# Kernel optimization log

Measured on AMD Instinct MI355X. Metric: run time of the kernel, lower is better.

Reference implementation:

```python
import jax, jax.numpy as jnp
import numpy as np

B = 4; IMG = 32; P = 2; C_IN = 3; H_DIM = 384; DEPTH = 8
GS = IMG // P; L = GS * GS
NSTATE = 16; KDIR = 4; DIN = 384; RANK = 24; MH = int(H_DIM * 4.0)
BOT = 128; NCLS = 1000; TFREQ = 256


def _silu(x):
    return x * jax.nn.sigmoid(x)


def _rms(x, w, eps=1e-6):
    return x * jax.lax.rsqrt(jnp.mean(x * x, -1, keepdims=True) + eps) * w


def _ln(x, w, b, eps=1e-5):
    mu = jnp.mean(x, -1, keepdims=True)
    v = jnp.mean((x - mu) ** 2, -1, keepdims=True)
    return (x - mu) * jax.lax.rsqrt(v + eps) * w + b


def _ln_na(x, eps=1e-6):
    mu = jnp.mean(x, -1, keepdims=True)
    v = jnp.mean((x - mu) ** 2, -1, keepdims=True)
    return (x - mu) * jax.lax.rsqrt(v + eps)


def _mod(x, shift, scale):
    return x * (1.0 + scale[:, None, :]) + shift[:, None, :]


def _ss2d(xin, in_w, conv_w, conv_b, xproj_w, dt_w, dt_b, A_logs, Ds, onorm_w, onorm_b, outp_w):
    Bb = xin.shape[0]
    z = xin @ in_w.T  # (B,L,DIN)
    z2d = z.reshape(Bb, GS, GS, DIN).transpose(0, 3, 1, 2)  # (B,DIN,H,W)
    z2d = jax.lax.conv_general_dilated(z2d, conv_w, (1, 1), 'SAME',
        feature_group_count=DIN, dimension_numbers=('NCHW', 'OIHW', 'NCHW'))
    z2d = _silu(z2d + conv_b[None, :, None, None])
    # cross_scan -> (B,K,DIN,L): row-major, reversed, col-major, reversed col-major
    s1 = z2d.reshape(Bb, DIN, L)
    s3 = z2d.transpose(0, 1, 3, 2).reshape(Bb, DIN, L)
    xs = jnp.stack([s1, s1[..., ::-1], s3, s3[..., ::-1]], axis=1)
    x_dbl = jnp.einsum('bkdl,kod->bkol', xs, xproj_w)
    dtr = x_dbl[:, :, :RANK]
    Bssm = x_dbl[:, :, RANK:RANK + NSTATE]   # (B,K,N,L)
    Cssm = x_dbl[:, :, RANK + NSTATE:]       # (B,K,N,L)
    dt = jnp.einsum('bkrl,kdr->bkdl', dtr, dt_w)
    dt = jax.nn.softplus(dt + dt_b[None, :, :, None])
    A = -jnp.exp(A_logs)                     # (K,DIN,N)
    dA = jnp.exp(jnp.einsum('bkdl,kdn->bkldn', dt, A))
    dBu = jnp.einsum('bkdl,bknl->bkldn', dt * xs, Bssm)
    def comb(e1, e2):
        a1, b1 = e1
        a2, b2 = e2
        return a1 * a2, a2 * b1 + b2
    _, hs = jax.lax.associative_scan(comb, (dA, dBu), axis=2)  # h over token axis
    ys = jnp.einsum('bkldn,bknl->bkdl', hs, Cssm) + Ds[None, :, :, None] * xs
    # cross_merge: undo each direction's reorder and sum
    m1 = ys[:, 0]
    m2 = ys[:, 1][..., ::-1]
    m3 = ys[:, 2].reshape(Bb, DIN, GS, GS).swapaxes(2, 3).reshape(Bb, DIN, L)
    m4 = ys[:, 3][..., ::-1].reshape(Bb, DIN, GS, GS).swapaxes(2, 3).reshape(Bb, DIN, L)
    out = (m1 + m2 + m3 + m4).transpose(0, 2, 1)  # (B,L,DIN)
    out = _ln(out, onorm_w, onorm_b)
    return out @ outp_w.T


def _forward(x, t, y, t_w1, t_b1, t_w2, t_b2, y_table, pe_w1, pe_w2, pe_b2, pos_embed,
             adaln_w, adaln_b, n1_w, n2_w, in_w, conv_w, conv_b, xproj_w, dt_w, dt_b,
             A_logs, Ds, onorm_w, onorm_b, outp_w, mlp_w1, mlp_b1, mlp_w2, mlp_b2,
             f_adaln_w, f_adaln_b, f_lin_w, f_lin_b):
    # timestep embedding (DiT TimestepEmbedder, freq dim 256)
    half = TFREQ // 2
    freqs = jnp.exp(-jnp.log(10000.0) * jnp.arange(half, dtype=jnp.float32) / half)
    ang = t[:, None] * freqs[None]
    temb = jnp.concatenate([jnp.cos(ang), jnp.sin(ang)], axis=-1)
    temb = _silu(temb @ t_w1.T + t_b1) @ t_w2.T + t_b2
    c = temb + y_table[y]  # (B,H_DIM)
    # bottleneck patch embed: patchify -> bottleneck linear -> hidden linear
    xp = x.reshape(B, C_IN, GS, P, GS, P).transpose(0, 2, 4, 1, 3, 5).reshape(B, L, C_IN * P * P)
    h = (xp @ pe_w1.T) @ pe_w2.T + pe_b2
    h = h + pos_embed
    for i in range(DEPTH):
        mod = _silu(c) @ adaln_w[i].T + adaln_b[i]
        sh1, sc1, g1, sh2, sc2, g2 = jnp.split(mod, 6, axis=-1)
        h = h + g1[:, None] * _ss2d(_mod(_rms(h, n1_w[i]), sh1, sc1),
            in_w[i], conv_w[i], conv_b[i], xproj_w[i], dt_w[i], dt_b[i],
            A_logs[i], Ds[i], onorm_w[i], onorm_b[i], outp_w[i])
        u = _mod(_rms(h, n2_w[i]), sh2, sc2)
        u12 = u @ mlp_w1[i].T + mlp_b1[i]
        u1, u2 = jnp.split(u12, 2, axis=-1)
        h = h + g2[:, None] * ((_silu(u1) * u2) @ mlp_w2[i].T + mlp_b2[i])
    modf = _silu(c) @ f_adaln_w.T + f_adaln_b
    shf, scf = jnp.split(modf, 2, axis=-1)
    h = _mod(_ln_na(h), shf, scf)
    out = h @ f_lin_w.T + f_lin_b  # (B,L,P*P*C_IN)
    out = out.reshape(B, GS, GS, P, P, C_IN)
    out = jnp.einsum('nhwpqc->nchpwq', out)
    return out.reshape(B, C_IN, IMG, IMG)


def _sincos_1d(dim, pos):
    omega = 1.0 / (10000.0 ** (np.arange(dim // 2, dtype=np.float64) / (dim / 2.0)))
    out = pos.reshape(-1)[:, None] * omega[None, :]
    return np.concatenate([np.sin(out), np.cos(out)], axis=1)


def _pos_embed_np(dim, gs):
    g = np.stack(np.meshgrid(np.arange(gs, dtype=np.float64), np.arange(gs, dtype=np.float64)), axis=0)
    return np.concatenate([_sincos_1d(dim // 2, g[0]), _sincos_1d(dim // 2, g[1])], axis=1).astype(np.float32)


def setup_inputs():
    key = jax.random.key(0)
    ks = iter(jax.random.split(key, 64))
    nrm = lambda shape, s=0.02: jax.random.normal(next(ks), shape, jnp.float32) * s
    d = {}
    d['x'] = jax.random.normal(next(ks), (B, C_IN, IMG, IMG), jnp.float32)
    d['t'] = jax.random.uniform(next(ks), (B,), jnp.float32) * 1000.0
    d['y'] = jax.random.randint(next(ks), (B,), 0, NCLS)
    d['t_w1'] = nrm((H_DIM, TFREQ)); d['t_b1'] = jnp.zeros((H_DIM,), jnp.float32)
    d['t_w2'] = nrm((H_DIM, H_DIM)); d['t_b2'] = jnp.zeros((H_DIM,), jnp.float32)
    d['y_table'] = nrm((NCLS, H_DIM))
    d['pe_w1'] = nrm((BOT, C_IN * P * P), 0.1)
    d['pe_w2'] = nrm((H_DIM, BOT), 0.1); d['pe_b2'] = jnp.zeros((H_DIM,), jnp.float32)
    d['pos_embed'] = jnp.asarray(_pos_embed_np(H_DIM, GS))[None]
    d['adaln_w'] = nrm((DEPTH, 6 * H_DIM, H_DIM)); d['adaln_b'] = jnp.zeros((DEPTH, 6 * H_DIM), jnp.float32)
    d['n1_w'] = jnp.ones((DEPTH, H_DIM), jnp.float32); d['n2_w'] = jnp.ones((DEPTH, H_DIM), jnp.float32)
    d['in_w'] = nrm((DEPTH, DIN, H_DIM), 0.05)
    d['conv_w'] = nrm((DEPTH, DIN, 1, 3, 3), 0.1); d['conv_b'] = jnp.zeros((DEPTH, DIN), jnp.float32)
    d['xproj_w'] = nrm((DEPTH, KDIR, RANK + 2 * NSTATE, DIN), 0.05)
    d['dt_w'] = nrm((DEPTH, KDIR, DIN, RANK), 0.1)
    d['dt_b'] = nrm((DEPTH, KDIR, DIN), 0.5)
    d['A_logs'] = jnp.tile(jnp.log(jnp.arange(1, NSTATE + 1, dtype=jnp.float32))[None, None, None, :], (DEPTH, KDIR, DIN, 1))
    d['Ds'] = jnp.ones((DEPTH, KDIR, DIN), jnp.float32)
    d['onorm_w'] = jnp.ones((DEPTH, DIN), jnp.float32); d['onorm_b'] = jnp.zeros((DEPTH, DIN), jnp.float32)
    d['outp_w'] = nrm((DEPTH, H_DIM, DIN), 0.05)
    d['mlp_w1'] = nrm((DEPTH, 2 * MH, H_DIM)); d['mlp_b1'] = jnp.zeros((DEPTH, 2 * MH), jnp.float32)
    d['mlp_w2'] = nrm((DEPTH, H_DIM, MH)); d['mlp_b2'] = jnp.zeros((DEPTH, H_DIM), jnp.float32)
    d['f_adaln_w'] = nrm((2 * H_DIM, H_DIM)); d['f_adaln_b'] = jnp.zeros((2 * H_DIM,), jnp.float32)
    d['f_lin_w'] = nrm((P * P * C_IN, H_DIM)); d['f_lin_b'] = jnp.zeros((P * P * C_IN,), jnp.float32)
    return d


def reference(x, t, y, t_w1, t_b1, t_w2, t_b2, y_table, pe_w1, pe_w2, pe_b2, pos_embed,
              adaln_w, adaln_b, n1_w, n2_w, in_w, conv_w, conv_b, xproj_w, dt_w, dt_b,
              A_logs, Ds, onorm_w, onorm_b, outp_w, mlp_w1, mlp_b1, mlp_w2, mlp_b2,
              f_adaln_w, f_adaln_b, f_lin_w, f_lin_b):
    return _forward(x, t, y, t_w1, t_b1, t_w2, t_b2, y_table, pe_w1, pe_w2, pe_b2, pos_embed,
                    adaln_w, adaln_b, n1_w, n2_w, in_w, conv_w, conv_b, xproj_w, dt_w, dt_b,
                    A_logs, Ds, onorm_w, onorm_b, outp_w, mlp_w1, mlp_b1, mlp_w2, mlp_b2,
                    f_adaln_w, f_adaln_b, f_lin_w, f_lin_b)
```

## Files before the change

### kernel.cpp

```cpp
#include <hip/hip_runtime.h>
#include <hip/hip_bf16.h>
#include <math.h>


#define DEV __device__ __forceinline__

typedef __bf16 bf16_t;
typedef __attribute__((ext_vector_type(8))) __bf16 bf16x8;
typedef __attribute__((ext_vector_type(4))) float f32x4;
typedef __attribute__((ext_vector_type(2))) _Float16 h2;

DEV float siluf(float x){ return x / (1.f + __expf(-x)); }
DEV float softplusf(float x){ return fmaxf(x, 0.f) + __logf(1.f + __expf(-fabsf(x))); }

DEV int perm_idx(int k, int l){
  switch(k & 3){
    case 0: return l;
    case 1: return 255 - l;
    case 2: return ((l & 15) << 4) | (l >> 4);
    default: { int r = 255 - l; return ((r & 15) << 4) | (r >> 4); }
  }
}

__global__ void k_cvt_layer(const float* __restrict__ inw, const float* __restrict__ outw,
                            const float* __restrict__ w1, const float* __restrict__ w2,
                            const float* __restrict__ xp, bf16_t* __restrict__ dst){
  int idx = (blockIdx.x*256 + threadIdx.x)*4;
  const float* src; int off;
  if (idx < 147456){ src = inw;  off = idx; }
  else if (idx < 294912){ src = outw; off = idx - 147456; }
  else if (idx < 1474560){
    int o = idx - 294912;
    int rowc = o / 384, col = o - rowc*384;
    int q = rowc >> 5, tt = rowc & 31;
    int srow = (tt < 16) ? (q*16 + tt) : (1536 + q*16 + (tt - 16));
    src = w1; off = srow*384 + col;
  }
  else if (idx < 2064384){ src = w2; off = idx - 1474560; }
  else { src = xp; off = idx - 2064384; }
  float4 v = *(const float4*)(src + off);
  union { bf16_t h[4]; uint2 u; } cv;
  cv.h[0] = (bf16_t)v.x; cv.h[1] = (bf16_t)v.y; cv.h[2] = (bf16_t)v.z; cv.h[3] = (bf16_t)v.w;
  *(uint2*)(dst + idx) = cv.u;
}

__global__ void k_cond(const float* __restrict__ t, const int* __restrict__ y,
                       const float* __restrict__ tw1, const float* __restrict__ tb1,
                       const float* __restrict__ tw2, const float* __restrict__ tb2,
                       const float* __restrict__ ytab, float* __restrict__ sc){
  int b = blockIdx.x; int o = threadIdx.x;
  __shared__ float temb[256]; __shared__ float h1[384];
  float tv = t[b];
  if (o < 128){
    float f = __expf(-logf(10000.f) * (float)o / 128.f);
    float a = tv * f;
    temb[o] = cosf(a); temb[128 + o] = sinf(a);
  }
  __syncthreads();
  float acc = tb1[o];
  for (int j = 0; j < 256; j++) acc += temb[j] * tw1[(size_t)o*256 + j];
  h1[o] = siluf(acc);
  __syncthreads();
  float acc2 = tb2[o];
  for (int j = 0; j < 384; j++) acc2 += h1[j] * tw2[(size_t)o*384 + j];
  float c = acc2 + ytab[(size_t)y[b]*384 + o];
  sc[b*384 + o] = siluf(c);
}

__global__ void k_patch(const float* __restrict__ x, const float* __restrict__ pw1,
                        const float* __restrict__ pw2, const float* __restrict__ pb2,
                        const float* __restrict__ pos, float* __restrict__ h){
  int bl = blockIdx.x; int b = bl >> 8; int l = bl & 255;
  int gh = l >> 4, gw = l & 15;
  __shared__ float xp[12]; __shared__ float tmp[128];
  int tid = threadIdx.x;
  if (tid < 12){
    int ci = tid >> 2, ph = (tid >> 1) & 1, pw = tid & 1;
    xp[tid] = x[((size_t)(b*3 + ci)*32 + gh*2 + ph)*32 + gw*2 + pw];
  }
  __syncthreads();
  if (tid < 128){
    float a = 0.f;
    #pragma unroll
    for (int k = 0; k < 12; k++) a += xp[k] * pw1[tid*12 + k];
    tmp[tid] = a;
  }
  __syncthreads();
  float a = pb2[tid];
  for (int j = 0; j < 128; j++) a += tmp[j] * pw2[(size_t)tid*128 + j];
  h[(size_t)(b*256 + l)*384 + tid] = a + pos[(size_t)l*384 + tid];
}

__global__ void k_lin_small(const float* __restrict__ sc, const float* __restrict__ W,
                            const float* __restrict__ bias, float* __restrict__ out, int N){
  int idx = blockIdx.x * blockDim.x + threadIdx.x;
  if (idx >= 4*N) return;
  int b = idx / N, o = idx % N;
  const float4* cp = (const float4*)(sc + b*384);
  const float4* wp = (const float4*)(W + (size_t)o*384);
  float a = bias[o];
  #pragma unroll 4
  for (int k = 0; k < 96; k++){
    float4 c4 = cp[k], w4 = wp[k];
    a += c4.x*w4.x + c4.y*w4.y + c4.z*w4.z + c4.w*w4.w;
  }
  out[idx] = a;
}

__global__ void k_rms_mod(const float* __restrict__ h, const float* __restrict__ nw,
                          const float* __restrict__ modBase, bf16_t* __restrict__ out){
  int bl = blockIdx.x; int b = bl >> 8;
  const float* hp = h + (size_t)bl*384;
  const float* mp = modBase + (size_t)b*18432;
  __shared__ float red[2];
  int tid = threadIdx.x;
  float v[3]; float ss = 0.f;
  #pragma unroll
  for (int ii = 0; ii < 3; ii++){ v[ii] = hp[tid + ii*128]; ss += v[ii]*v[ii]; }
  #pragma unroll
  for (int off = 32; off; off >>= 1) ss += __shfl_down(ss, off);
  if ((tid & 63) == 0) red[tid >> 6] = ss;
  __syncthreads();
  ss = red[0] + red[1];
  float inv = rsqrtf(ss / 384.f + 1e-6f);
  #pragma unroll
  for (int ii = 0; ii < 3; ii++){
    int d = tid + ii*128;
    float xv = v[ii] * inv * nw[d];
    out[(size_t)bl*384 + d] = (bf16_t)(xv * (1.f + mp[384 + d]) + mp[d]);
  }
}

template<int MODE>
__global__ __launch_bounds__(256) void k_gemm_bf(
    const bf16_t* __restrict__ A, const bf16_t* __restrict__ W,
    const float* __restrict__ bias, float* __restrict__ C,
    const float* __restrict__ modBase, int N, int K, int Nstore){
  __shared__ bf16_t As[2][64*40];
  __shared__ bf16_t Ws[2][64*40];
  const int tid = threadIdx.x;
  const int bm = blockIdx.y * 64, bn = blockIdx.x * 64;
  const int wave = tid >> 6, lane = tid & 63;
  const int m16 = lane & 15, kg = lane >> 4;
  const int r = tid >> 2, seg = tid & 3;
  const int nt = K / 32;

  uint4 aP, wP;
  auto loadT = [&](int kt){
    wP = *(const uint4*)(W + (size_t)(bn + r)*K + kt*32 + seg*8);
    aP = *(const uint4*)(A + (size_t)(bm + r)*K + kt*32 + seg*8);
  };
  auto stash = [&](int buf){
    *(uint4*)&As[buf][r*40 + seg*8] = aP;
    *(uint4*)&Ws[buf][r*40 + seg*8] = wP;
  };

  f32x4 acc[4] = {};
  loadT(0); stash(0); __syncthreads();
  for (int kt = 0; kt < nt; kt++){
    int buf = kt & 1;
    if (kt + 1 < nt) loadT(kt + 1);
    bf16x8 af = *(bf16x8*)&As[buf][(wave*16 + m16)*40 + kg*8];
    #pragma unroll
    for (int j = 0; j < 4; j++){
      bf16x8 bfr = *(bf16x8*)&Ws[buf][(j*16 + m16)*40 + kg*8];
      acc[j] = __builtin_amdgcn_mfma_f32_16x16x32_bf16(af, bfr, acc[j], 0, 0, 0);
    }
    if (kt + 1 < nt) stash(buf ^ 1);
    __syncthreads();
  }

  if constexpr (MODE == 4){
    bf16_t* Cb = (bf16_t*)C;
    const int Np = N >> 1;
    #pragma unroll
    for (int jp = 0; jp < 2; jp++){
      int pcol = (bn >> 1) + jp*16 + m16;
      float b1v = bias[pcol], b2v = bias[Np + pcol];
      #pragma unroll
      for (int rg = 0; rg < 4; rg++){
        int row = bm + wave*16 + kg*4 + rg;
        float u1v = acc[jp*2][rg] + b1v;
        float u2v = acc[jp*2 + 1][rg] + b2v;
        Cb[(size_t)row*Np + pcol] = (bf16_t)(siluf(u1v)*u2v);
      }
    }
  } else {
    #pragma unroll
    for (int j = 0; j < 4; j++){
      int col = bn + j*16 + m16;
      if (col < Nstore){
        #pragma unroll
        for (int rg = 0; rg < 4; rg++){
          int row = bm + wave*16 + kg*4 + rg;
          float v = acc[j][rg];
          if constexpr (MODE == 5) v += bias[col];
          if constexpr (MODE == 2 || MODE == 5)
            C[(size_t)row*N + col] += modBase[(size_t)(row >> 8)*18432 + col] * v;
          else
            C[(size_t)row*N + col] = v;
        }
      }
    }
  }
}

__global__ void k_conv(const float* __restrict__ z, const float* __restrict__ cw,
                       const float* __restrict__ cb, float* __restrict__ convT,
                       bf16_t* __restrict__ convB){
  int bl = blockIdx.x; int b = bl >> 8, l = bl & 255;
  int hh = l >> 4, ww = l & 15;
  int d = threadIdx.x;
  float acc = cb[d];
  #pragma unroll
  for (int kh = 0; kh < 3; kh++){
    int yy = hh + kh - 1; if ((unsigned)yy > 15u) continue;
    #pragma unroll
    for (int kw = 0; kw < 3; kw++){
      int xx = ww + kw - 1; if ((unsigned)xx > 15u) continue;
      acc += z[(size_t)(b*256 + yy*16 + xx)*384 + d] * cw[d*9 + kh*3 + kw];
    }
  }
  float s = siluf(acc);
  convT[(size_t)bl*384 + d] = s;
  convB[(size_t)bl*384 + d] = (bf16_t)s;
}

__global__ __launch_bounds__(256) void k_scan(
    const float* __restrict__ xdblS, const float* __restrict__ convT,
    const float* __restrict__ dtw, const float* __restrict__ dtb,
    const float* __restrict__ Alog, const float* __restrict__ Dsw,
    float* __restrict__ ysT){
  int blk = blockIdx.x;
  int d = blk % 384; int k = (blk / 384) & 3; int b = blk / 1536;
  int tid = threadIdx.x;
  int n = tid & 15, chunk = tid >> 4;
  __shared__ float sdt[256], sxv[256], sy[256];
  __shared__ float sA[16][17], sB[16][17], sPre[16][17];
  __shared__ _Float16 sB16[256*18];
  __shared__ _Float16 sC16[256*18];

  {
    int l = tid;
    int lp = perm_idx(k, l);
    const float* row = xdblS + (size_t)(b*256 + lp)*224 + k*56;
    const float4* xr = (const float4*)(row);
    const float4* w  = (const float4*)(dtw + ((size_t)k*384 + d)*24);
    float a0 = dtb[k*384 + d];
    #pragma unroll
    for (int r4 = 0; r4 < 6; r4++){
      float4 xv4 = xr[r4], wv4 = w[r4];
      a0 += xv4.x*wv4.x + xv4.y*wv4.y + xv4.z*wv4.z + xv4.w*wv4.w;
    }
    sdt[l] = softplusf(a0);
    sxv[l] = convT[(size_t)(b*256 + lp)*384 + d];
    const float4* bp = (const float4*)(row + 24);
    h2* bl = (h2*)(sB16 + l*18);
    h2* cl = (h2*)(sC16 + l*18);
    #pragma unroll
    for (int q = 0; q < 4; q++){
      float4 bv = bp[q];
      h2 p0; p0[0] = (_Float16)bv.x; p0[1] = (_Float16)bv.y;
      h2 p1; p1[0] = (_Float16)bv.z; p1[1] = (_Float16)bv.w;
      bl[q*2] = p0; bl[q*2+1] = p1;
      float4 cv = bp[q+4];
      h2 q0; q0[0] = (_Float16)cv.x; q0[1] = (_Float16)cv.y;
      h2 q1; q1[0] = (_Float16)cv.z; q1[1] = (_Float16)cv.w;
      cl[q*2] = q0; cl[q*2+1] = q1;
    }
  }
  __syncthreads();

  float a = -__expf(Alog[((size_t)(k*384) + d)*16 + n]);
  float Dv = Dsw[k*384 + d];

  float dA[16], dBu[16];
  float Ap = 1.f, hloc = 0.f;
  #pragma unroll
  for (int i = 0; i < 16; i++){
    int l = chunk*16 + i;
    float dtv = sdt[l];
    float e = __expf(dtv * a);
    float u = dtv * sxv[l] * (float)sB16[l*18 + n];
    dA[i] = e; dBu[i] = u;
    Ap *= e; hloc = e*hloc + u;
  }
  sA[chunk][n] = Ap; sB[chunk][n] = hloc;
  __syncthreads();

  if (tid < 16){
    float carry = 0.f;
    #pragma unroll
    for (int c = 0; c < 16; c++){
      sPre[c][tid] = carry;
      carry = sA[c][tid]*carry + sB[c][tid];
    }
  }
  __syncthreads();

  float h = sPre[chunk][n];
  #pragma unroll
  for (int i = 0; i < 16; i++){
    int l = chunk*16 + i;
    h = dA[i]*h + dBu[i];
    float p = h * (float)sC16[l*18 + n];
    p += __shfl_xor(p, 1);
    p += __shfl_xor(p, 2);
    p += __shfl_xor(p, 4);
    p += __shfl_xor(p, 8);
    if (n == 0) sy[l] = p + Dv * sxv[l];
  }
  __syncthreads();
  ysT[((size_t)(b*4 + k)*384 + d)*256 + tid] = sy[tid];
}

__global__ void k_merge_ln(const float* __restrict__ ysT, const float* __restrict__ ow,
                           const float* __restrict__ ob, bf16_t* __restrict__ out){
  int bl = blockIdx.x; int b = bl >> 8; int l = bl & 255;
  int tl = ((l & 15) << 4) | (l >> 4);
  int i2 = 255 - l, i4 = 255 - tl;
  __shared__ float red[4];
  int tid = threadIdx.x;
  const float* base = ysT + (size_t)b*4*384*256;
  float v[3]; float s = 0.f, s2 = 0.f;
  #pragma unroll
  for (int ii = 0; ii < 3; ii++){
    int d = tid + ii*128;
    float vv = base[(size_t)d*256 + l]
             + base[(size_t)(384 + d)*256 + i2]
             + base[(size_t)(768 + d)*256 + tl]
             + base[(size_t)(1152 + d)*256 + i4];
    v[ii] = vv; s += vv; s2 += vv*vv;
  }
  #pragma unroll
  for (int off = 32; off; off >>= 1){ s += __shfl_down(s, off); s2 += __shfl_down(s2, off); }
  if ((tid & 63) == 0){ red[tid >> 6] = s; red[2 + (tid >> 6)] = s2; }
  __syncthreads();
  s = red[0] + red[1]; s2 = red[2] + red[3];
  float mu = s / 384.f;
  float var = s2 / 384.f - mu*mu;
  float inv = rsqrtf(var + 1e-5f);
  #pragma unroll
  for (int ii = 0; ii < 3; ii++){
    int d = tid + ii*128;
    out[(size_t)bl*384 + d] = (bf16_t)((v[ii] - mu) * inv * ow[d] + ob[d]);
  }
}

__global__ void k_final(const float* __restrict__ h, const float* __restrict__ modf,
                        const float* __restrict__ flw, const float* __restrict__ flb,
                        float* __restrict__ out){
  int bl = blockIdx.x; int b = bl >> 8; int l = bl & 255;
  int tid = threadIdx.x;
  __shared__ float buf[384]; __shared__ float red[4];
  const float* hp = h + (size_t)bl*384;
  float v[3]; float s = 0.f, s2 = 0.f;
  #pragma unroll
  for (int ii = 0; ii < 3; ii++){ float xv = hp[tid + ii*128]; v[ii] = xv; s += xv; s2 += xv*xv; }
  #pragma unroll
  for (int off = 32; off; off >>= 1){ s += __shfl_down(s, off); s2 += __shfl_down(s2, off); }
  if ((tid & 63) == 0){ red[tid >> 6] = s; red[2 + (tid >> 6)] = s2; }
  __syncthreads();
  s = red[0] + red[1]; s2 = red[2] + red[3];
  float mu = s / 384.f;
  float var = s2 / 384.f - mu*mu;
  float inv = rsqrtf(var + 1e-6f);
  #pragma unroll
  for (int ii = 0; ii < 3; ii++){
    int d = tid + ii*128;
    buf[d] = (v[ii] - mu) * inv * (1.f + modf[b*768 + 384 + d]) + modf[b*768 + d];
  }
  __syncthreads();
  if (tid < 12){
    float a = flb[tid];
    for (int k = 0; k < 384; k++) a += buf[k] * flw[(size_t)tid*384 + k];
    int p = tid / 6, q = (tid / 3) & 1, cc = tid % 3;
    int gh = l >> 4, gw = l & 15;
    out[((size_t)(b*3 + cc)*32 + gh*2 + p)*32 + gw*2 + q] = a;
  }
}

extern "C" void kernel_launch(void* const* d_in, const int* in_sizes, int n_in,
                              void* d_out, int out_size, void* d_ws, size_t ws_size,
                              hipStream_t stream){
  const float* x       = (const float*)d_in[0];
  const float* t       = (const float*)d_in[1];
  const int*   y       = (const int*)  d_in[2];
  const float* t_w1    = (const float*)d_in[3];
  const float* t_b1    = (const float*)d_in[4];
  const float* t_w2    = (const float*)d_in[5];
  const float* t_b2    = (const float*)d_in[6];
  const float* y_table = (const float*)d_in[7];
  const float* pe_w1   = (const float*)d_in[8];
  const float* pe_w2   = (const float*)d_in[9];
  const float* pe_b2   = (const float*)d_in[10];
  const float* pos     = (const float*)d_in[11];
  const float* adaln_w = (const float*)d_in[12];
  const float* adaln_b = (const float*)d_in[13];
  const float* n1_w    = (const float*)d_in[14];
  const float* n2_w    = (const float*)d_in[15];
  const float* in_w    = (const float*)d_in[16];
  const float* conv_w  = (const float*)d_in[17];
  const float* conv_b  = (const float*)d_in[18];
  const float* xproj_w = (const float*)d_in[19];
  const float* dt_w    = (const float*)d_in[20];
  const float* dt_b    = (const float*)d_in[21];
  const float* A_logs  = (const float*)d_in[22];
  const float* Ds      = (const float*)d_in[23];
  const float* onorm_w = (const float*)d_in[24];
  const float* onorm_b = (const float*)d_in[25];
  const float* outp_w  = (const float*)d_in[26];
  const float* mlp_w1  = (const float*)d_in[27];
  const float* mlp_b1  = (const float*)d_in[28];
  const float* mlp_w2  = (const float*)d_in[29];
  const float* mlp_b2  = (const float*)d_in[30];
  const float* f_adaln_w = (const float*)d_in[31];
  const float* f_adaln_b = (const float*)d_in[32];
  const float* f_lin_w = (const float*)d_in[33];
  const float* f_lin_b = (const float*)d_in[34];

  float* ws = (float*)d_ws;
  float*  sc      = ws + 0;
  float*  h       = ws + 1536;
  float*  modAll  = ws + 394752;
  float*  modf    = ws + 468480;
  float*  buf1    = ws + 471552;
  float*  convT   = ws + 864768;
  float*  xdblS   = ws + 1257984;
  float*  u12     = ws + 1487360;
  float*  ysT     = ws + 4633088;
  bf16_t* xin_bf  = (bf16_t*)(ws + 6205952);
  bf16_t* ssin_bf = (bf16_t*)(ws + 6402560);
  bf16_t* conv_bf = (bf16_t*)(ws + 6599168);
  bf16_t* wbf     = (bf16_t*)(ws + 6795776);
  bf16_t* u12b    = (bf16_t*)u12;

  bf16_t* wbf_in = wbf;
  bf16_t* wbf_out = wbf + 147456;
  bf16_t* wbf_w1 = wbf + 294912;
  bf16_t* wbf_w2 = wbf + 1474560;
  bf16_t* wbf_xp = wbf + 2064384;

  k_cond<<<dim3(4), dim3(384), 0, stream>>>(t, y, t_w1, t_b1, t_w2, t_b2, y_table, sc);
  k_patch<<<dim3(1024), dim3(384), 0, stream>>>(x, pe_w1, pe_w2, pe_b2, pos, h);
  k_lin_small<<<dim3(288), dim3(256), 0, stream>>>(sc, adaln_w, adaln_b, modAll, 18432);

  for (int i = 0; i < 8; i++){
    const float* modL = modAll + (size_t)i*2304;
    k_cvt_layer<<<dim3(2100), dim3(256), 0, stream>>>(
        in_w + (size_t)i*147456, outp_w + (size_t)i*147456, mlp_w1 + (size_t)i*1179648,
        mlp_w2 + (size_t)i*589824, xproj_w + (size_t)i*86016, wbf);
    k_rms_mod<<<dim3(1024), dim3(128), 0, stream>>>(h, n1_w + i*384, modL + 0, xin_bf);
    k_gemm_bf<0><<<dim3(6,16), dim3(256), 0, stream>>>(
        xin_bf, wbf_in, nullptr, buf1, nullptr, 384, 384, 384);
    k_conv<<<dim3(1024), dim3(384), 0, stream>>>(
        buf1, conv_w + (size_t)i*384*9, conv_b + i*384, convT, conv_bf);
    k_gemm_bf<0><<<dim3(4,16), dim3(256), 0, stream>>>(
        conv_bf, wbf_xp, nullptr, xdblS, nullptr, 224, 384, 224);
    k_scan<<<dim3(6144), dim3(256), 0, stream>>>(
        xdblS, convT, dt_w + (size_t)i*4*384*24, dt_b + (size_t)i*4*384,
        A_logs + (size_t)i*4*384*16, Ds + (size_t)i*4*384, ysT);
    k_merge_ln<<<dim3(1024), dim3(128), 0, stream>>>(
        ysT, onorm_w + i*384, onorm_b + i*384, ssin_bf);
    k_gemm_bf<2><<<dim3(6,16), dim3(256), 0, stream>>>(
        ssin_bf, wbf_out, nullptr, h, modL + 768, 384, 384, 384);
    k_rms_mod<<<dim3(1024), dim3(128), 0, stream>>>(h, n2_w + i*384, modL + 1152, xin_bf);
    k_gemm_bf<4><<<dim3(48,16), dim3(256), 0, stream>>>(
        xin_bf, wbf_w1, mlp_b1 + (size_t)i*3072, (float*)u12b, nullptr, 3072, 384, 3072);
    k_gemm_bf<5><<<dim3(6,16), dim3(256), 0, stream>>>(
        u12b, wbf_w2, mlp_b2 + (size_t)i*384, h, modL + 1920, 384, 1536, 384);
  }

  k_lin_small<<<dim3(12), dim3(256), 0, stream>>>(sc, f_adaln_w, f_adaln_b, modf, 768);
  k_final<<<dim3(1024), dim3(128), 0, stream>>>(h, modf, f_lin_w, f_lin_b, (float*)d_out);
}
```

Measured before the change: 1.307 ms.

## Convert all layer weights once and process two channels per scan block

Weight conversion to bf16 now runs as one large launch for all 8 layers before the loop, provided the workspace is big enough, replacing eight per-layer conversion launches. The workspace is repacked so each layer's converted weights have their own slot. The selective scan kernel now handles two DIN channels per block, halving the grid. This lets the B/C fp16 staging, the xdbl row loads and the chunk-carry structure be shared across both channels, at the cost of more registers per thread.

```diff
diff --git a/kernel.cpp b/kernel.cpp
--- a/kernel.cpp
+++ b/kernel.cpp
@@ -22,10 +22,8 @@
   }
 }
 
-__global__ void k_cvt_layer(const float* __restrict__ inw, const float* __restrict__ outw,
-                            const float* __restrict__ w1, const float* __restrict__ w2,
-                            const float* __restrict__ xp, bf16_t* __restrict__ dst){
-  int idx = (blockIdx.x*256 + threadIdx.x)*4;
+DEV void cvt_one(int idx, const float* inw, const float* outw, const float* w1,
+                 const float* w2, const float* xp, bf16_t* dst){
   const float* src; int off;
   if (idx < 147456){ src = inw;  off = idx; }
   else if (idx < 294912){ src = outw; off = idx - 147456; }
@@ -42,6 +40,24 @@
   union { bf16_t h[4]; uint2 u; } cv;
   cv.h[0] = (bf16_t)v.x; cv.h[1] = (bf16_t)v.y; cv.h[2] = (bf16_t)v.z; cv.h[3] = (bf16_t)v.w;
   *(uint2*)(dst + idx) = cv.u;
+}
+
+__global__ void k_cvt_layer(const float* __restrict__ inw, const float* __restrict__ outw,
+                            const float* __restrict__ w1, const float* __restrict__ w2,
+                            const float* __restrict__ xp, bf16_t* __restrict__ dst){
+  int idx = (blockIdx.x*256 + threadIdx.x)*4;
+  cvt_one(idx, inw, outw, w1, w2, xp, dst);
+}
+
+__global__ void k_cvt_all(const float* __restrict__ inw, const float* __restrict__ outw,
+                          const float* __restrict__ w1, const float* __restrict__ w2,
+                          const float* __restrict__ xp, bf16_t* __restrict__ dst){
+  int layer = blockIdx.x / 2100;
+  int within = blockIdx.x % 2100;
+  int idx = (within*256 + threadIdx.x)*4;
+  cvt_one(idx, inw + (size_t)layer*147456, outw + (size_t)layer*147456,
+          w1 + (size_t)layer*1179648, w2 + (size_t)layer*589824,
+          xp + (size_t)layer*86016, dst + (size_t)layer*2150400);
 }
 
 __global__ void k_cond(const float* __restrict__ t, const int* __restrict__ y,
@@ -232,11 +248,12 @@
     const float* __restrict__ Alog, const float* __restrict__ Dsw,
     float* __restrict__ ysT){
   int blk = blockIdx.x;
-  int d = blk % 384; int k = (blk / 384) & 3; int b = blk / 1536;
+  int dp = blk % 192; int k = (blk / 192) & 3; int b = blk / 768;
+  int d0 = dp*2;
   int tid = threadIdx.x;
   int n = tid & 15, chunk = tid >> 4;
-  __shared__ float sdt[256], sxv[256], sy[256];
-  __shared__ float sA[16][17], sB[16][17], sPre[16][17];
+  __shared__ float sdt[2][256], sxv[2][256], sy[2][256];
+  __shared__ float sA[2][16][17], sBc[2][16][17], sPre[2][16][17];
   __shared__ _Float16 sB16[256*18];
   __shared__ _Float16 sC16[256*18];
 
@@ -245,15 +262,22 @@
     int lp = perm_idx(k, l);
     const float* row = xdblS + (size_t)(b*256 + lp)*224 + k*56;
     const float4* xr = (const float4*)(row);
-    const float4* w  = (const float4*)(dtw + ((size_t)k*384 + d)*24);
-    float a0 = dtb[k*384 + d];
-    #pragma unroll
-    for (int r4 = 0; r4 < 6; r4++){
-      float4 xv4 = xr[r4], wv4 = w[r4];
-      a0 += xv4.x*wv4.x + xv4.y*wv4.y + xv4.z*wv4.z + xv4.w*wv4.w;
-    }
-    sdt[l] = softplusf(a0);
-    sxv[l] = convT[(size_t)(b*256 + lp)*384 + d];
+    float4 x0 = xr[0], x1 = xr[1], x2 = xr[2], x3 = xr[3], x4 = xr[4], x5 = xr[5];
+    #pragma unroll
+    for (int j = 0; j < 2; j++){
+      const float4* w = (const float4*)(dtw + ((size_t)k*384 + d0 + j)*24);
+      float4 w0 = w[0], w1 = w[1], w2 = w[2], w3 = w[3], w4 = w[4], w5 = w[5];
+      float a0 = dtb[k*384 + d0 + j];
+      a0 += x0.x*w0.x + x0.y*w0.y + x0.z*w0.z + x0.w*w0.w;
+      a0 += x1.x*w1.x + x1.y*w1.y + x1.z*w1.z + x1.w*w1.w;
+      a0 += x2.x*w2.x + x2.y*w2.y + x2.z*w2.z + x2.w*w2.w;
+      a0 += x3.x*w3.x + x3.y*w3.y + x3.z*w3.z + x3.w*w3.w;
+      a0 += x4.x*w4.x + x4.y*w4.y + x4.z*w4.z + x4.w*w4.w;
+      a0 += x5.x*w5.x + x5.y*w5.y + x5.z*w5.z + x5.w*w5.w;
+      sdt[j][l] = softplusf(a0);
+    }
+    float2 xv2 = *(const float2*)(convT + (size_t)(b*256 + lp)*384 + d0);
+    sxv[0][l] = xv2.x; sxv[1][l] = xv2.y;
     const float4* bp = (const float4*)(row + 24);
     h2* bl = (h2*)(sB16 + l*18);
     h2* cl = (h2*)(sC16 + l*18);
@@ -271,47 +295,63 @@
   }
   __syncthreads();
 
-  float a = -__expf(Alog[((size_t)(k*384) + d)*16 + n]);
-  float Dv = Dsw[k*384 + d];
-
-  float dA[16], dBu[16];
-  float Ap = 1.f, hloc = 0.f;
+  float av[2], Dv[2];
+  #pragma unroll
+  for (int j = 0; j < 2; j++){
+    av[j] = -__expf(Alog[((size_t)(k*384) + d0 + j)*16 + n]);
+    Dv[j] = Dsw[k*384 + d0 + j];
+  }
+
+  float dA[2][16], dBu[2][16];
+  float Ap[2] = {1.f, 1.f}, hl[2] = {0.f, 0.f};
   #pragma unroll
   for (int i = 0; i < 16; i++){
     int l = chunk*16 + i;
-    float dtv = sdt[l];
-    float e = __expf(dtv * a);
-    float u = dtv * sxv[l] * (float)sB16[l*18 + n];
-    dA[i] = e; dBu[i] = u;
-    Ap *= e; hloc = e*hloc + u;
-  }
-  sA[chunk][n] = Ap; sB[chunk][n] = hloc;
-  __syncthreads();
-
-  if (tid < 16){
+    float bn16 = (float)sB16[l*18 + n];
+    #pragma unroll
+    for (int j = 0; j < 2; j++){
+      float dtv = sdt[j][l];
+      float e = __expf(dtv * av[j]);
+      float u = dtv * sxv[j][l] * bn16;
+      dA[j][i] = e; dBu[j][i] = u;
+      Ap[j] *= e; hl[j] = e*hl[j] + u;
+    }
+  }
+  #pragma unroll
+  for (int j = 0; j < 2; j++){ sA[j][chunk][n] = Ap[j]; sBc[j][chunk][n] = hl[j]; }
+  __syncthreads();
+
+  if (tid < 32){
+    int j = tid >> 4, nn = tid & 15;
     float carry = 0.f;
     #pragma unroll
     for (int c = 0; c < 16; c++){
-      sPre[c][tid] = carry;
-      carry = sA[c][tid]*carry + sB[c][tid];
-    }
-  }
-  __syncthreads();
-
-  float h = sPre[chunk][n];
+      sPre[j][c][nn] = carry;
+      carry = sA[j][c][nn]*carry + sBc[j][c][nn];
+    }
+  }
+  __syncthreads();
+
+  float hh[2] = {sPre[0][chunk][n], sPre[1][chunk][n]};
   #pragma unroll
   for (int i = 0; i < 16; i++){
     int l = chunk*16 + i;
-    h = dA[i]*h + dBu[i];
-    float p = h * (float)sC16[l*18 + n];
-    p += __shfl_xor(p, 1);
-    p += __shfl_xor(p, 2);
-    p += __shfl_xor(p, 4);
-    p += __shfl_xor(p, 8);
-    if (n == 0) sy[l] = p + Dv * sxv[l];
-  }
-  __syncthreads();
-  ysT[((size_t)(b*4 + k)*384 + d)*256 + tid] = sy[tid];
+    float cn = (float)sC16[l*18 + n];
+    hh[0] = dA[0][i]*hh[0] + dBu[0][i];
+    hh[1] = dA[1][i]*hh[1] + dBu[1][i];
+    float p0 = hh[0]*cn, p1 = hh[1]*cn;
+    p0 += __shfl_xor(p0, 1); p1 += __shfl_xor(p1, 1);
+    p0 += __shfl_xor(p0, 2); p1 += __shfl_xor(p1, 2);
+    p0 += __shfl_xor(p0, 4); p1 += __shfl_xor(p1, 4);
+    p0 += __shfl_xor(p0, 8); p1 += __shfl_xor(p1, 8);
+    if (n == 0){
+      sy[0][l] = p0 + Dv[0]*sxv[0][l];
+      sy[1][l] = p1 + Dv[1]*sxv[1][l];
+    }
+  }
+  __syncthreads();
+  ysT[((size_t)(b*4 + k)*384 + d0)*256 + tid] = sy[0][tid];
+  ysT[((size_t)(b*4 + k)*384 + d0 + 1)*256 + tid] = sy[1][tid];
 }
 
 __global__ void k_merge_ln(const float* __restrict__ ysT, const float* __restrict__ ow,
@@ -427,29 +467,35 @@
   float*  buf1    = ws + 471552;
   float*  convT   = ws + 864768;
   float*  xdblS   = ws + 1257984;
-  float*  u12     = ws + 1487360;
-  float*  ysT     = ws + 4633088;
-  bf16_t* xin_bf  = (bf16_t*)(ws + 6205952);
-  bf16_t* ssin_bf = (bf16_t*)(ws + 6402560);
-  bf16_t* conv_bf = (bf16_t*)(ws + 6599168);
-  bf16_t* wbf     = (bf16_t*)(ws + 6795776);
-  bf16_t* u12b    = (bf16_t*)u12;
-
-  bf16_t* wbf_in = wbf;
-  bf16_t* wbf_out = wbf + 147456;
-  bf16_t* wbf_w1 = wbf + 294912;
-  bf16_t* wbf_w2 = wbf + 1474560;
-  bf16_t* wbf_xp = wbf + 2064384;
+  bf16_t* u12b    = (bf16_t*)(ws + 1487360);
+  float*  ysT     = ws + 2273792;
+  bf16_t* xin_bf  = (bf16_t*)(ws + 3846656);
+  bf16_t* ssin_bf = (bf16_t*)(ws + 4043264);
+  bf16_t* conv_bf = (bf16_t*)(ws + 4239872);
+  bf16_t* wbfBase = (bf16_t*)(ws + 4436480);
+
+  const bool bigws = ws_size >= (size_t)13038080 * 4;
 
   k_cond<<<dim3(4), dim3(384), 0, stream>>>(t, y, t_w1, t_b1, t_w2, t_b2, y_table, sc);
   k_patch<<<dim3(1024), dim3(384), 0, stream>>>(x, pe_w1, pe_w2, pe_b2, pos, h);
   k_lin_small<<<dim3(288), dim3(256), 0, stream>>>(sc, adaln_w, adaln_b, modAll, 18432);
+  if (bigws)
+    k_cvt_all<<<dim3(16800), dim3(256), 0, stream>>>(
+        in_w, outp_w, mlp_w1, mlp_w2, xproj_w, wbfBase);
 
   for (int i = 0; i < 8; i++){
     const float* modL = modAll + (size_t)i*2304;
-    k_cvt_layer<<<dim3(2100), dim3(256), 0, stream>>>(
-        in_w + (size_t)i*147456, outp_w + (size_t)i*147456, mlp_w1 + (size_t)i*1179648,
-        mlp_w2 + (size_t)i*589824, xproj_w + (size_t)i*86016, wbf);
+    bf16_t* wbf = bigws ? wbfBase + (size_t)i*2150400 : wbfBase;
+    if (!bigws)
+      k_cvt_layer<<<dim3(2100), dim3(256), 0, stream>>>(
+          in_w + (size_t)i*147456, outp_w + (size_t)i*147456, mlp_w1 + (size_t)i*1179648,
+          mlp_w2 + (size_t)i*589824, xproj_w + (size_t)i*86016, wbf);
+    bf16_t* wbf_in  = wbf;
+    bf16_t* wbf_out = wbf + 147456;
+    bf16_t* wbf_w1  = wbf + 294912;
+    bf16_t* wbf_w2  = wbf + 1474560;
+    bf16_t* wbf_xp  = wbf + 2064384;
+
     k_rms_mod<<<dim3(1024), dim3(128), 0, stream>>>(h, n1_w + i*384, modL + 0, xin_bf);
     k_gemm_bf<0><<<dim3(6,16), dim3(256), 0, stream>>>(
         xin_bf, wbf_in, nullptr, buf1, nullptr, 384, 384, 384);
@@ -457,7 +503,7 @@
         buf1, conv_w + (size_t)i*384*9, conv_b + i*384, convT, conv_bf);
     k_gemm_bf<0><<<dim3(4,16), dim3(256), 0, stream>>>(
         conv_bf, wbf_xp, nullptr, xdblS, nullptr, 224, 384, 224);
-    k_scan<<<dim3(6144), dim3(256), 0, stream>>>(
+    k_scan<<<dim3(3072), dim3(256), 0, stream>>>(
         xdblS, convT, dt_w + (size_t)i*4*384*24, dt_b + (size_t)i*4*384,
         A_logs + (size_t)i*4*384*16, Ds + (size_t)i*4*384, ysT);
     k_merge_ln<<<dim3(1024), dim3(128), 0, stream>>>(
```

Measured after the change: 1.177 ms. 1.11x faster.
